# Performance work log

Measured on AMD Instinct MI355X. Metric: run time of the kernel, lower is better.

Reference implementation:

```python
import jax, jax.numpy as jnp
import numpy as np
import math

B, S, H, A = 128, 2048, 512, 512

def setup_inputs() -> dict:
    key = jax.random.key(0)
    k1, k2, k3 = jax.random.split(key, 3)
    return {
        "lstm_output": jax.random.normal(k1, (B, S, H), dtype=jnp.float32),
        "w_omega": jax.random.normal(k2, (H, A), dtype=jnp.float32) * (1.0 / math.sqrt(2 * H)),
        "b_omega": jnp.zeros((A,), dtype=jnp.float32),
        "u_omega": jax.random.normal(k3, (A,), dtype=jnp.float32) * (1.0 / math.sqrt(A)),
    }

def reference(lstm_output, w_omega, b_omega, u_omega):
    # v: [B, S, A] = tanh(x @ W + b) / sqrt(A)
    scale = math.sqrt(w_omega.shape[1])
    v = jnp.tanh(jnp.einsum('bsh,ha->bsa', lstm_output, w_omega) + b_omega) / scale
    vu = jnp.einsum('bsa,a->bs', v, u_omega)  # [B, S]
    max_vu = jnp.max(vu, axis=1, keepdims=True)
    exp_vu = jnp.exp(vu - max_vu)
    alphas = exp_vu / (jnp.sum(exp_vu, axis=1, keepdims=True) + 1e-10)  # [B, S]
    output = jnp.einsum('bs,bsh->bh', alphas, lstm_output)  # [B, H]
    return (output, alphas)
```

## Files before the change

### kernel.cpp

```cpp
#include <hip/hip_runtime.h>
#include <hip/hip_bf16.h>
#include <math.h>


#define M_TOK 262144
#define HDIM 512
#define ADIM 512
#define SDIM 2048
#define BDIM 128

#define WSWZ_FLOATS 131072
#define PART_STRIDE 514
#define NCHUNK 4096

typedef __attribute__((ext_vector_type(8))) short short8;
typedef __attribute__((ext_vector_type(4))) float f32x4;

static __device__ __forceinline__ unsigned short f2bf(float f) {
    unsigned u = __builtin_bit_cast(unsigned, f);
    unsigned rnd = 0x7FFFu + ((u >> 16) & 1u);
    return (unsigned short)((u + rnd) >> 16);
}

__global__ void k_wswz(const float* __restrict__ W, unsigned short* __restrict__ Wswz) {
    int t = blockIdx.x * 256 + threadIdx.x;
    int lane = t & 63;
    int frag = t >> 6;
    int kb = frag >> 5;
    int nb = frag & 31;
    int n  = nb * 16 + (lane & 15);
    int k0 = kb * 32 + (lane >> 4) * 8;
    short8 s;
#pragma unroll
    for (int j = 0; j < 8; ++j)
        s[j] = (short)f2bf(W[(k0 + j) * ADIM + n]);
    reinterpret_cast<short8*>(Wswz)[t] = s;
}

__global__ __launch_bounds__(256, 2)
void k_gemm_fused(const float* __restrict__ X, const unsigned short* __restrict__ Wswz,
                  const float* __restrict__ bvec, const float* __restrict__ u,
                  float* __restrict__ vu, float* __restrict__ part) {
    __shared__ __align__(16) unsigned short Xs[64][520];
    __shared__ float vured[4][64];
    __shared__ float e_lds[64];

    const int tid  = threadIdx.x;
    const int lane = tid & 63;
    const int wave = tid >> 6;
    const int lm   = lane & 15;
    const int quad = lane >> 4;
    const int r0   = blockIdx.x * 64;
    float* pblk    = part + (size_t)blockIdx.x * PART_STRIDE;

    const float4* Xp = reinterpret_cast<const float4*>(X + (size_t)r0 * HDIM);
#pragma unroll 8
    for (int it = 0; it < 32; ++it) {
        int idx  = it * 256 + tid;
        int row  = idx >> 7;
        int col4 = idx & 127;
        float4 v = Xp[idx];
        unsigned lo = (unsigned)f2bf(v.x) | ((unsigned)f2bf(v.y) << 16);
        unsigned hi = (unsigned)f2bf(v.z) | ((unsigned)f2bf(v.w) << 16);
        unsigned* d = reinterpret_cast<unsigned*>(&Xs[row][col4 * 4]);
        d[0] = lo; d[1] = hi;
    }
    __syncthreads();

    const short8* wbl = reinterpret_cast<const short8*>(Wswz) + lane + wave * 512;

    f32x4 acc[4][8];
#pragma unroll
    for (int i = 0; i < 4; ++i)
#pragma unroll
        for (int j = 0; j < 8; ++j)
            acc[i][j] = (f32x4){0.f, 0.f, 0.f, 0.f};

    short8 bcur[8], bnxt[8];
#pragma unroll
    for (int j = 0; j < 8; ++j) bcur[j] = wbl[j * 64];

    for (int kb = 0; kb < 16; ++kb) {
        if (kb < 15) {
#pragma unroll
            for (int j = 0; j < 8; ++j) bnxt[j] = wbl[(kb + 1) * 2048 + j * 64];
        }
        short8 a[4];
#pragma unroll
        for (int i = 0; i < 4; ++i)
            a[i] = *reinterpret_cast<const short8*>(&Xs[i * 16 + lm][kb * 32 + quad * 8]);
#pragma unroll
        for (int i = 0; i < 4; ++i)
#pragma unroll
            for (int j = 0; j < 8; ++j)
                acc[i][j] = __builtin_amdgcn_mfma_f32_16x16x32_bf16(a[i], bcur[j], acc[i][j], 0, 0, 0);
#pragma unroll
        for (int j = 0; j < 8; ++j) bcur[j] = bnxt[j];
    }

    float vus[16];
#pragma unroll
    for (int q = 0; q < 16; ++q) vus[q] = 0.f;
    const int colbase = wave * 128 + lm;
#pragma unroll
    for (int j = 0; j < 8; ++j) {
        int col  = colbase + j * 16;
        float uu = u[col];
        float bb = bvec[col];
#pragma unroll
        for (int i = 0; i < 4; ++i)
#pragma unroll
            for (int r = 0; r < 4; ++r) {
                float x = acc[i][j][r] + bb;
                float e = __expf(2.0f * x);
                float t = 1.0f - 2.0f / (e + 1.0f);
                vus[i * 4 + r] += t * uu;
            }
    }
#pragma unroll
    for (int m = 1; m <= 8; m <<= 1) {
#pragma unroll
        for (int q = 0; q < 16; ++q)
            vus[q] += __shfl_xor(vus[q], m, 64);
    }
    if (lm == 0) {
#pragma unroll
        for (int i = 0; i < 4; ++i)
#pragma unroll
            for (int r = 0; r < 4; ++r)
                vured[wave][i * 16 + quad * 4 + r] = vus[i * 4 + r];
    }
    __syncthreads();

    if (tid < 64) {
        float v = (vured[0][tid] + vured[1][tid] + vured[2][tid] + vured[3][tid])
                  * 0.044194173824159216f;
        vu[r0 + tid] = v;
        float m = v;
#pragma unroll
        for (int j = 1; j <= 32; j <<= 1) m = fmaxf(m, __shfl_xor(m, j, 64));
        float e = __expf(v - m);
        e_lds[tid] = e;
        float l = e;
#pragma unroll
        for (int j = 1; j <= 32; j <<= 1) l += __shfl_xor(l, j, 64);
        if (tid == 0) { pblk[512] = m; pblk[513] = l; }
    }
    __syncthreads();

    float o0 = 0.f, o1 = 0.f;
    const int c2 = tid * 2;
#pragma unroll 8
    for (int s = 0; s < 64; ++s) {
        unsigned uu = *reinterpret_cast<const unsigned*>(&Xs[s][c2]);
        float e  = e_lds[s];
        float xl = __builtin_bit_cast(float, uu << 16);
        float xh = __builtin_bit_cast(float, uu & 0xFFFF0000u);
        o0 = fmaf(e, xl, o0);
        o1 = fmaf(e, xh, o1);
    }
    *reinterpret_cast<float2*>(&pblk[c2]) = make_float2(o0, o1);
}

__global__ __launch_bounds__(256)
void k_combine(const float* __restrict__ part, float* __restrict__ out,
               float* __restrict__ params) {
    const int b = blockIdx.x, tid = threadIdx.x;
    __shared__ float wch[32];
    __shared__ float sinv;
    const float* pb = part + (size_t)b * 32 * PART_STRIDE;
    if (tid < 32) {
        float m = pb[tid * PART_STRIDE + 512];
        float l = pb[tid * PART_STRIDE + 513];
        float M = m;
#pragma unroll
        for (int j = 1; j <= 16; j <<= 1) M = fmaxf(M, __shfl_xor(M, j, 32));
        float w  = __expf(m - M);
        float lw = l * w;
#pragma unroll
        for (int j = 1; j <= 16; j <<= 1) lw += __shfl_xor(lw, j, 32);
        wch[tid] = w;
        if (tid == 0) {
            float inv = 1.0f / (lw + 1e-10f);
            sinv = inv;
            params[b] = M;
            params[BDIM + b] = inv;
        }
    }
    __syncthreads();
    float inv = sinv;
    float o0 = 0.f, o1 = 0.f;
    const int h = tid * 2;
#pragma unroll 8
    for (int c = 0; c < 32; ++c) {
        float w = wch[c];
        float2 v = *reinterpret_cast<const float2*>(&pb[c * PART_STRIDE + h]);
        o0 = fmaf(w, v.x, o0);
        o1 = fmaf(w, v.y, o1);
    }
    out[b * HDIM + h]     = o0 * inv;
    out[b * HDIM + h + 1] = o1 * inv;
}

__global__ void k_alphas(float* __restrict__ vu, const float* __restrict__ params) {
    int i = blockIdx.x * 256 + threadIdx.x;
    int b = i >> 11;
    vu[i] = __expf(vu[i] - params[b]) * params[BDIM + b];
}

extern "C" void kernel_launch(void* const* d_in, const int* in_sizes, int n_in,
                              void* d_out, int out_size, void* d_ws, size_t ws_size,
                              hipStream_t stream) {
    const float* X  = (const float*)d_in[0];
    const float* W  = (const float*)d_in[1];
    const float* bb = (const float*)d_in[2];
    const float* u  = (const float*)d_in[3];
    float* out = (float*)d_out;

    unsigned short* Wswz = (unsigned short*)d_ws;
    float* part   = (float*)d_ws + WSWZ_FLOATS;
    float* params = (float*)d_ws + WSWZ_FLOATS + NCHUNK * PART_STRIDE;

    k_wswz<<<128, 256, 0, stream>>>(W, Wswz);
    k_gemm_fused<<<NCHUNK, 256, 0, stream>>>(X, Wswz, bb, u, out + 65536, part);
    k_combine<<<BDIM, 256, 0, stream>>>(part, out, params);
    k_alphas<<<M_TOK / 256, 256, 0, stream>>>(out + 65536, params);
}
```

Measured before the change: 798.9 us.

## Make GEMM blocks persistent over 8 chunks with double-buffered X prefetch

Each GEMM block now handles 8 consecutive 64-row chunks with 512 threads (8 waves, each covering 64 output columns). The next chunk's X is prefetched into registers and converted into a second LDS buffer while the current chunk computes, so global load latency overlaps MFMA work. The weighted-sum stage is split across two halves of the block. The alphas normalization is folded into the combine kernel, removing one launch. The cost is heavy register pressure from the 16 float4 staging registers and doubled LDS, which may cut occupancy, plus a grid of only 512 blocks.

Result: slower. 1.136 ms (+42.2%).

```diff
diff --git a/kernel.cpp b/kernel.cpp
--- a/kernel.cpp
+++ b/kernel.cpp
@@ -12,6 +12,8 @@
 #define WSWZ_FLOATS 131072
 #define PART_STRIDE 514
 #define NCHUNK 4096
+#define NCPB 8
+#define GEMM_BLOCKS (NCHUNK / NCPB)
 
 typedef __attribute__((ext_vector_type(8))) short short8;
 typedef __attribute__((ext_vector_type(4))) float f32x4;
@@ -37,137 +39,178 @@
     reinterpret_cast<short8*>(Wswz)[t] = s;
 }
 
-__global__ __launch_bounds__(256, 2)
+__global__ __launch_bounds__(512, 2)
 void k_gemm_fused(const float* __restrict__ X, const unsigned short* __restrict__ Wswz,
                   const float* __restrict__ bvec, const float* __restrict__ u,
                   float* __restrict__ vu, float* __restrict__ part) {
-    __shared__ __align__(16) unsigned short Xs[64][520];
-    __shared__ float vured[4][64];
+    __shared__ __align__(16) unsigned short Xs[2][64][520];
+    __shared__ float vured[8][64];
     __shared__ float e_lds[64];
+    __shared__ float opart[512];
 
     const int tid  = threadIdx.x;
     const int lane = tid & 63;
     const int wave = tid >> 6;
     const int lm   = lane & 15;
     const int quad = lane >> 4;
-    const int r0   = blockIdx.x * 64;
-    float* pblk    = part + (size_t)blockIdx.x * PART_STRIDE;
-
-    const float4* Xp = reinterpret_cast<const float4*>(X + (size_t)r0 * HDIM);
-#pragma unroll 8
-    for (int it = 0; it < 32; ++it) {
-        int idx  = it * 256 + tid;
+    const int chunk0 = blockIdx.x * NCPB;
+
+    const float4* Xp = reinterpret_cast<const float4*>(X) + (size_t)chunk0 * 8192;
+
+    float4 st[16];
+
+#pragma unroll
+    for (int t = 0; t < 16; ++t) st[t] = Xp[t * 512 + tid];
+#pragma unroll
+    for (int t = 0; t < 16; ++t) {
+        int idx  = t * 512 + tid;
         int row  = idx >> 7;
         int col4 = idx & 127;
-        float4 v = Xp[idx];
-        unsigned lo = (unsigned)f2bf(v.x) | ((unsigned)f2bf(v.y) << 16);
-        unsigned hi = (unsigned)f2bf(v.z) | ((unsigned)f2bf(v.w) << 16);
-        unsigned* d = reinterpret_cast<unsigned*>(&Xs[row][col4 * 4]);
-        d[0] = lo; d[1] = hi;
-    }
+        uint2 d;
+        d.x = (unsigned)f2bf(st[t].x) | ((unsigned)f2bf(st[t].y) << 16);
+        d.y = (unsigned)f2bf(st[t].z) | ((unsigned)f2bf(st[t].w) << 16);
+        *reinterpret_cast<uint2*>(&Xs[0][row][col4 * 4]) = d;
+    }
+#pragma unroll
+    for (int t = 0; t < 16; ++t) st[t] = Xp[8192 + t * 512 + tid];
     __syncthreads();
 
-    const short8* wbl = reinterpret_cast<const short8*>(Wswz) + lane + wave * 512;
-
-    f32x4 acc[4][8];
-#pragma unroll
-    for (int i = 0; i < 4; ++i)
-#pragma unroll
-        for (int j = 0; j < 8; ++j)
-            acc[i][j] = (f32x4){0.f, 0.f, 0.f, 0.f};
-
-    short8 bcur[8], bnxt[8];
-#pragma unroll
-    for (int j = 0; j < 8; ++j) bcur[j] = wbl[j * 64];
-
-    for (int kb = 0; kb < 16; ++kb) {
-        if (kb < 15) {
-#pragma unroll
-            for (int j = 0; j < 8; ++j) bnxt[j] = wbl[(kb + 1) * 2048 + j * 64];
-        }
-        short8 a[4];
+    const short8* wbl = reinterpret_cast<const short8*>(Wswz) + wave * 256 + lane;
+
+    for (int c = 0; c < NCPB; ++c) {
+        const int cur = c & 1;
+
+        f32x4 acc[4][4];
 #pragma unroll
         for (int i = 0; i < 4; ++i)
-            a[i] = *reinterpret_cast<const short8*>(&Xs[i * 16 + lm][kb * 32 + quad * 8]);
-#pragma unroll
-        for (int i = 0; i < 4; ++i)
-#pragma unroll
-            for (int j = 0; j < 8; ++j)
-                acc[i][j] = __builtin_amdgcn_mfma_f32_16x16x32_bf16(a[i], bcur[j], acc[i][j], 0, 0, 0);
-#pragma unroll
-        for (int j = 0; j < 8; ++j) bcur[j] = bnxt[j];
-    }
-
-    float vus[16];
-#pragma unroll
-    for (int q = 0; q < 16; ++q) vus[q] = 0.f;
-    const int colbase = wave * 128 + lm;
-#pragma unroll
-    for (int j = 0; j < 8; ++j) {
-        int col  = colbase + j * 16;
-        float uu = u[col];
-        float bb = bvec[col];
-#pragma unroll
-        for (int i = 0; i < 4; ++i)
-#pragma unroll
-            for (int r = 0; r < 4; ++r) {
-                float x = acc[i][j][r] + bb;
-                float e = __expf(2.0f * x);
-                float t = 1.0f - 2.0f / (e + 1.0f);
-                vus[i * 4 + r] += t * uu;
-            }
-    }
-#pragma unroll
-    for (int m = 1; m <= 8; m <<= 1) {
-#pragma unroll
-        for (int q = 0; q < 16; ++q)
-            vus[q] += __shfl_xor(vus[q], m, 64);
-    }
-    if (lm == 0) {
-#pragma unroll
-        for (int i = 0; i < 4; ++i)
-#pragma unroll
-            for (int r = 0; r < 4; ++r)
-                vured[wave][i * 16 + quad * 4 + r] = vus[i * 4 + r];
-    }
-    __syncthreads();
-
-    if (tid < 64) {
-        float v = (vured[0][tid] + vured[1][tid] + vured[2][tid] + vured[3][tid])
-                  * 0.044194173824159216f;
-        vu[r0 + tid] = v;
-        float m = v;
-#pragma unroll
-        for (int j = 1; j <= 32; j <<= 1) m = fmaxf(m, __shfl_xor(m, j, 64));
-        float e = __expf(v - m);
-        e_lds[tid] = e;
-        float l = e;
-#pragma unroll
-        for (int j = 1; j <= 32; j <<= 1) l += __shfl_xor(l, j, 64);
-        if (tid == 0) { pblk[512] = m; pblk[513] = l; }
-    }
-    __syncthreads();
-
-    float o0 = 0.f, o1 = 0.f;
-    const int c2 = tid * 2;
+#pragma unroll
+            for (int j = 0; j < 4; ++j)
+                acc[i][j] = (f32x4){0.f, 0.f, 0.f, 0.f};
+
+        short8 bcur[4], bnxt[4];
+#pragma unroll
+        for (int j = 0; j < 4; ++j) bcur[j] = wbl[j * 64];
+
+        for (int kb = 0; kb < 16; ++kb) {
+            if (kb < 15) {
+#pragma unroll
+                for (int j = 0; j < 4; ++j) bnxt[j] = wbl[(kb + 1) * 2048 + j * 64];
+            }
+            short8 a[4];
+#pragma unroll
+            for (int i = 0; i < 4; ++i)
+                a[i] = *reinterpret_cast<const short8*>(&Xs[cur][i * 16 + lm][kb * 32 + quad * 8]);
+#pragma unroll
+            for (int i = 0; i < 4; ++i)
+#pragma unroll
+                for (int j = 0; j < 4; ++j)
+                    acc[i][j] = __builtin_amdgcn_mfma_f32_16x16x32_bf16(a[i], bcur[j], acc[i][j], 0, 0, 0);
+#pragma unroll
+            for (int j = 0; j < 4; ++j) bcur[j] = bnxt[j];
+        }
+
+        if (c + 1 < NCPB) {
+#pragma unroll
+            for (int t = 0; t < 16; ++t) {
+                int idx  = t * 512 + tid;
+                int row  = idx >> 7;
+                int col4 = idx & 127;
+                uint2 d;
+                d.x = (unsigned)f2bf(st[t].x) | ((unsigned)f2bf(st[t].y) << 16);
+                d.y = (unsigned)f2bf(st[t].z) | ((unsigned)f2bf(st[t].w) << 16);
+                *reinterpret_cast<uint2*>(&Xs[cur ^ 1][row][col4 * 4]) = d;
+            }
+        }
+        if (c + 2 < NCPB) {
+            const float4* Xp2 = Xp + (size_t)(c + 2) * 8192;
+#pragma unroll
+            for (int t = 0; t < 16; ++t) st[t] = Xp2[t * 512 + tid];
+        }
+
+        float vus[16];
+#pragma unroll
+        for (int q = 0; q < 16; ++q) vus[q] = 0.f;
+#pragma unroll
+        for (int j = 0; j < 4; ++j) {
+            int col  = wave * 64 + j * 16 + lm;
+            float uu = u[col];
+            float bb = bvec[col];
+#pragma unroll
+            for (int i = 0; i < 4; ++i)
+#pragma unroll
+                for (int r = 0; r < 4; ++r) {
+                    float x = acc[i][j][r] + bb;
+                    float e = __expf(2.0f * x);
+                    float t = 1.0f - 2.0f / (e + 1.0f);
+                    vus[i * 4 + r] += t * uu;
+                }
+        }
+#pragma unroll
+        for (int m = 1; m <= 8; m <<= 1) {
+#pragma unroll
+            for (int q = 0; q < 16; ++q)
+                vus[q] += __shfl_xor(vus[q], m, 64);
+        }
+        if (lm == 0) {
+#pragma unroll
+            for (int i = 0; i < 4; ++i)
+#pragma unroll
+                for (int r = 0; r < 4; ++r)
+                    vured[wave][i * 16 + quad * 4 + r] = vus[i * 4 + r];
+        }
+        __syncthreads();
+
+        const int chunk = chunk0 + c;
+        float* pblk = part + (size_t)chunk * PART_STRIDE;
+        if (tid < 64) {
+            float v = (vured[0][tid] + vured[1][tid] + vured[2][tid] + vured[3][tid] +
+                       vured[4][tid] + vured[5][tid] + vured[6][tid] + vured[7][tid])
+                      * 0.044194173824159216f;
+            vu[chunk * 64 + tid] = v;
+            float m = v;
+#pragma unroll
+            for (int j = 1; j <= 32; j <<= 1) m = fmaxf(m, __shfl_xor(m, j, 64));
+            float e = __expf(v - m);
+            e_lds[tid] = e;
+            float l = e;
+#pragma unroll
+            for (int j = 1; j <= 32; j <<= 1) l += __shfl_xor(l, j, 64);
+            if (tid == 0) { pblk[512] = m; pblk[513] = l; }
+        }
+        __syncthreads();
+
+        {
+            const int half = tid >> 8;
+            const int c2   = (tid & 255) * 2;
+            const int s0   = half * 32;
+            float o0 = 0.f, o1 = 0.f;
 #pragma unroll 8
-    for (int s = 0; s < 64; ++s) {
-        unsigned uu = *reinterpret_cast<const unsigned*>(&Xs[s][c2]);
-        float e  = e_lds[s];
-        float xl = __builtin_bit_cast(float, uu << 16);
-        float xh = __builtin_bit_cast(float, uu & 0xFFFF0000u);
-        o0 = fmaf(e, xl, o0);
-        o1 = fmaf(e, xh, o1);
-    }
-    *reinterpret_cast<float2*>(&pblk[c2]) = make_float2(o0, o1);
+            for (int s = 0; s < 32; ++s) {
+                unsigned uu = *reinterpret_cast<const unsigned*>(&Xs[cur][s0 + s][c2]);
+                float e  = e_lds[s0 + s];
+                float xl = __builtin_bit_cast(float, uu << 16);
+                float xh = __builtin_bit_cast(float, uu & 0xFFFF0000u);
+                o0 = fmaf(e, xl, o0);
+                o1 = fmaf(e, xh, o1);
+            }
+            if (half) { opart[c2] = o0; opart[c2 + 1] = o1; }
+            __syncthreads();
+            if (!half) {
+                o0 += opart[c2];
+                o1 += opart[c2 + 1];
+                *reinterpret_cast<float2*>(&pblk[c2]) = make_float2(o0, o1);
+            }
+        }
+        __syncthreads();
+    }
 }
 
 __global__ __launch_bounds__(256)
-void k_combine(const float* __restrict__ part, float* __restrict__ out,
-               float* __restrict__ params) {
+void k_finish(const float* __restrict__ part, float* __restrict__ out,
+              float* __restrict__ alphas) {
     const int b = blockIdx.x, tid = threadIdx.x;
     __shared__ float wch[32];
-    __shared__ float sinv;
+    __shared__ float sM, sI;
     const float* pb = part + (size_t)b * 32 * PART_STRIDE;
     if (tid < 32) {
         float m = pb[tid * PART_STRIDE + 512];
@@ -180,15 +223,11 @@
 #pragma unroll
         for (int j = 1; j <= 16; j <<= 1) lw += __shfl_xor(lw, j, 32);
         wch[tid] = w;
-        if (tid == 0) {
-            float inv = 1.0f / (lw + 1e-10f);
-            sinv = inv;
-            params[b] = M;
-            params[BDIM + b] = inv;
-        }
+        if (tid == 0) { sM = M; sI = 1.0f / (lw + 1e-10f); }
     }
     __syncthreads();
-    float inv = sinv;
+    const float M = sM, inv = sI;
+
     float o0 = 0.f, o1 = 0.f;
     const int h = tid * 2;
 #pragma unroll 8
@@ -200,12 +239,17 @@
     }
     out[b * HDIM + h]     = o0 * inv;
     out[b * HDIM + h + 1] = o1 * inv;
-}
-
-__global__ void k_alphas(float* __restrict__ vu, const float* __restrict__ params) {
-    int i = blockIdx.x * 256 + threadIdx.x;
-    int b = i >> 11;
-    vu[i] = __expf(vu[i] - params[b]) * params[BDIM + b];
+
+    float4* ab = reinterpret_cast<float4*>(alphas + (size_t)b * SDIM);
+#pragma unroll
+    for (int k = 0; k < 2; ++k) {
+        float4 v = ab[tid + k * 256];
+        v.x = __expf(v.x - M) * inv;
+        v.y = __expf(v.y - M) * inv;
+        v.z = __expf(v.z - M) * inv;
+        v.w = __expf(v.w - M) * inv;
+        ab[tid + k * 256] = v;
+    }
 }
 
 extern "C" void kernel_launch(void* const* d_in, const int* in_sizes, int n_in,
@@ -218,11 +262,9 @@
     float* out = (float*)d_out;
 
     unsigned short* Wswz = (unsigned short*)d_ws;
-    float* part   = (float*)d_ws + WSWZ_FLOATS;
-    float* params = (float*)d_ws + WSWZ_FLOATS + NCHUNK * PART_STRIDE;
+    float* part = (float*)d_ws + WSWZ_FLOATS;
 
     k_wswz<<<128, 256, 0, stream>>>(W, Wswz);
-    k_gemm_fused<<<NCHUNK, 256, 0, stream>>>(X, Wswz, bb, u, out + 65536, part);
-    k_combine<<<BDIM, 256, 0, stream>>>(part, out, params);
-    k_alphas<<<M_TOK / 256, 256, 0, stream>>>(out + 65536, params);
-}
+    k_gemm_fused<<<GEMM_BLOCKS, 512, 0, stream>>>(X, Wswz, bb, u, out + 65536, part);
+    k_finish<<<BDIM, 256, 0, stream>>>(part, out, out + 65536);
+}
```
